# Kernel tuning notes

Measured on AMD Instinct MI355X. Metric: run time of the kernel, lower is better.

The kernel has to match this reference:

```python
import jax, jax.numpy as jnp
import numpy as np

B, T, C = 2, 2048, 2048
NH = 16          # n_head
G = 4            # group_size
NKV = NH // G    # kv heads
HD = C // NH     # head_dim = 128
BASE = 10000.0


def setup_inputs() -> dict:
    key = jax.random.key(0)
    ks = jax.random.split(key, 9)
    s = 0.02
    return {
        "x": jax.random.normal(ks[0], (B, T, C), jnp.float32),
        "wq_w": jax.random.normal(ks[1], (C, C), jnp.float32) * s,
        "wq_b": jax.random.normal(ks[2], (C,), jnp.float32) * s,
        "wk_w": jax.random.normal(ks[3], (C // G, C), jnp.float32) * s,
        "wk_b": jax.random.normal(ks[4], (C // G,), jnp.float32) * s,
        "wv_w": jax.random.normal(ks[5], (C // G, C), jnp.float32) * s,
        "wv_b": jax.random.normal(ks[6], (C // G,), jnp.float32) * s,
        "cp_w": jax.random.normal(ks[7], (C, C), jnp.float32) * s,
        "cp_b": jax.random.normal(ks[8], (C,), jnp.float32) * s,
    }


def _rope(x):
    # Faithful to source: RoPE is applied to [B, H, T, HD] but the module
    # reads seq_len = x.size(1) == H, so the rotation angle is indexed by the
    # HEAD axis and broadcast over sequence positions.
    b, h, t, d = x.shape
    half = d // 2
    theta = 1.0 / (BASE ** (jnp.arange(0, half, dtype=jnp.float32) * 2.0 / d))  # [half]
    ang = jnp.arange(h, dtype=jnp.float32)[:, None] * theta[None, :]            # [h, half]
    cos = jnp.cos(ang)[None, :, None, :]  # [1, h, 1, half]
    sin = jnp.sin(ang)[None, :, None, :]
    xs = x.reshape(b, h, t, half, 2)
    x0, x1 = xs[..., 0], xs[..., 1]
    out = jnp.stack([x0 * cos - x1 * sin, x1 * cos + x0 * sin], axis=-1)
    return out.reshape(b, h, t, d)


def reference(x, wq_w, wq_b, wk_w, wk_b, wv_w, wv_b, cp_w, cp_b):
    b, t, c = x.shape
    q = x @ wq_w.T + wq_b                                  # [B,T,C]
    k = x @ wk_w.T + wk_b                                  # [B,T,C//G]
    v = x @ wv_w.T + wv_b                                  # [B,T,C//G]
    q = q.reshape(b, t, NH, HD).transpose(0, 2, 1, 3)      # [B,NH,T,HD]
    k = k.reshape(b, t, NKV, HD).transpose(0, 2, 1, 3)     # [B,NKV,T,HD]
    v = v.reshape(b, t, NKV, HD).transpose(0, 2, 1, 3)
    q = _rope(q)
    k = _rope(k)
    # GQA expand: each kv head repeated G times consecutively
    k = jnp.repeat(k, G, axis=1)                           # [B,NH,T,HD]
    v = jnp.repeat(v, G, axis=1)
    att = jnp.einsum('bhqd,bhkd->bhqk', q, k) / (HD ** 0.5)
    mask = jnp.tril(jnp.ones((t, t), dtype=bool))
    att = jnp.where(mask[None, None], att, -jnp.inf)
    att = jax.nn.softmax(att, axis=-1)
    y = jnp.einsum('bhqk,bhkd->bhqd', att, v)
    y = y.transpose(0, 2, 1, 3).reshape(b, t, c)
    return y @ cp_w.T + cp_b
```

## Files before the change

kernel.cpp:

```cpp
#include <hip/hip_runtime.h>

typedef unsigned short u16;
typedef __bf16 bf16x8 __attribute__((ext_vector_type(8)));
typedef float f32x4 __attribute__((ext_vector_type(4)));
typedef float f32x16 __attribute__((ext_vector_type(16)));
typedef unsigned u32x4 __attribute__((ext_vector_type(4)));

#define T_   2048
#define C_   2048
#define HD_  128
#define NH_  16
#define NKV_ 4
#define M_   4096

typedef __attribute__((address_space(1))) const void* as1_cvp;
typedef __attribute__((address_space(3))) void* as3_vp;

__device__ __forceinline__ void gload16(const void* g, void* l) {
  __builtin_amdgcn_global_load_lds((as1_cvp)g, (as3_vp)l, 16, 0, 0);
}

__device__ __forceinline__ u16 f2bf(float f) {
  unsigned u = __builtin_bit_cast(unsigned, f);
  return (u16)((u + 0x7fffu + ((u >> 16) & 1u)) >> 16);
}

__device__ __forceinline__ float fexp2(float x) {
  float r;
  asm("v_exp_f32 %0, %1" : "=v"(r) : "v"(x));
  return r;
}

__device__ __forceinline__ unsigned cvtpk(float a, float b) {
  unsigned d;
  asm("v_cvt_pk_bf16_f32 %0, %1, %2" : "=v"(d) : "v"(a), "v"(b));
  return d;
}

__global__ void cvt_bf16(const float4* __restrict__ in, ushort4* __restrict__ out, int n4) {
  int i = blockIdx.x * blockDim.x + threadIdx.x;
  if (i >= n4) return;
  float4 v = in[i];
  ushort4 r;
  r.x = f2bf(v.x); r.y = f2bf(v.y); r.z = f2bf(v.z); r.w = f2bf(v.w);
  out[i] = r;
}

__global__ void copy_f32(const float* __restrict__ in, float* __restrict__ out, int n) {
  int i = blockIdx.x * blockDim.x + threadIdx.x;
  if (i < n) out[i] = in[i];
}

__global__ void rope_fold_w(const float* __restrict__ W, u16* __restrict__ out, int npair) {
  int idx = blockIdx.x * blockDim.x + threadIdx.x;
  int p  = idx >> 9;
  int c4 = (idx & 511) << 2;
  if (p >= npair) return;
  int h  = p >> 6;
  int ii = p & 63;
  float theta = __expf(-(float)ii * (9.210340371976184f / 64.0f));
  float s, c;
  __sincosf((float)h * theta, &s, &c);
  size_t r0 = (size_t)(2 * p) * 2048 + c4;
  size_t r1 = r0 + 2048;
  float4 a = *(const float4*)(W + r0);
  float4 b = *(const float4*)(W + r1);
  ushort4 o0, o1;
  o0.x = f2bf(a.x * c - b.x * s); o0.y = f2bf(a.y * c - b.y * s);
  o0.z = f2bf(a.z * c - b.z * s); o0.w = f2bf(a.w * c - b.w * s);
  o1.x = f2bf(b.x * c + a.x * s); o1.y = f2bf(b.y * c + a.y * s);
  o1.z = f2bf(b.z * c + a.z * s); o1.w = f2bf(b.w * c + a.w * s);
  *(ushort4*)(out + r0) = o0;
  *(ushort4*)(out + r1) = o1;
}

__global__ void rope_fold_b(const float* __restrict__ bin, float* __restrict__ bout, int npair) {
  int p = blockIdx.x * blockDim.x + threadIdx.x;
  if (p >= npair) return;
  int h = p >> 6, ii = p & 63;
  float theta = __expf(-(float)ii * (9.210340371976184f / 64.0f));
  float s, c;
  __sincosf((float)h * theta, &s, &c);
  float a = bin[2 * p], b = bin[2 * p + 1];
  bout[2 * p]     = a * c - b * s;
  bout[2 * p + 1] = b * c + a * s;
}

template<int BN, int MODE>
__global__ __launch_bounds__(512)
void gemm11(const u16* __restrict__ A, const u16* __restrict__ W,
            const float* __restrict__ bias, void* __restrict__ op0,
            void* __restrict__ op1, void* __restrict__ op2, const float qscale) {
  constexpr int NREP = BN / 32;
  constexpr int ABUF = 16384;
  constexpr int BBUF = BN * 64;
  constexpr int NBL  = BN / 64;
  __shared__ __align__(16) u16 sm[3 * ABUF + 2 * BBUF];
  const int tid  = threadIdx.x;
  const int lane = tid & 63;
  const int wid  = tid >> 6;
  const int wr = wid >> 1, wc = wid & 1;
  const int m0 = blockIdx.y << 8;
  const int n0 = blockIdx.x * BN;
  const int K  = C_;
  const int fr = lane & 15, g = lane >> 4;
  const int rs0 = ((g ^ (fr & 7)) << 3);
  const int rs1 = (((4 + g) ^ (fr & 7)) << 3);

  size_t sofA[4]; int sdstA[4];
#pragma unroll
  for (int l = 0; l < 4; ++l) {
    const int j = l * 512 + tid, rl = j >> 3, sl = j & 7;
    sofA[l] = (size_t)rl * K + ((sl ^ (rl & 7)) << 3);
    sdstA[l] = j * 8;
  }
  size_t sofB[NBL]; int sdstB[NBL];
#pragma unroll
  for (int l = 0; l < NBL; ++l) {
    const int j = l * 512 + tid, rl = j >> 3, sl = j & 7;
    sofB[l] = (size_t)rl * K + ((sl ^ (rl & 7)) << 3);
    sdstB[l] = j * 8;
  }
  const u16* Ab = A + (size_t)m0 * K;
  const u16* Bb = W + (size_t)n0 * K;

  f32x4 acc[4][NREP] = {};

#define SA(l, ks, buf) gload16(Ab + (size_t)(ks) * 64 + sofA[l], sm + (buf) * ABUF + sdstA[l]);
#define SB(l, ks, buf) gload16(Bb + (size_t)(ks) * 64 + sofB[l], sm + 3 * ABUF + (buf) * BBUF + sdstB[l]);

#pragma unroll
  for (int l = 0; l < NBL; ++l) SB(l, 0, 0)
#pragma unroll
  for (int l = 0; l < 4; ++l) SA(l, 0, 0)
#pragma unroll
  for (int l = 0; l < 4; ++l) SA(l, 1, 1)
  asm volatile("s_waitcnt vmcnt(4)" ::: "memory");
  __builtin_amdgcn_s_barrier();
  __builtin_amdgcn_sched_barrier(0);

  int a0 = 0, a2 = 2;
  for (int s = 0; s < 32; ++s) {
    const int ab = a0 * ABUF;
    const int bb = 3 * ABUF + (s & 1) * BBUF;
    const int b1 = (s & 1) ^ 1;
    bf16x8 af0[4], af1[4], bq0[NREP], bq1[NREP];
#pragma unroll
    for (int ni = 0; ni < NREP; ++ni)
      bq0[ni] = *(const bf16x8*)&sm[bb + (wc * (BN / 2) + ni * 16 + fr) * 64 + rs0];
#pragma unroll
    for (int mi = 0; mi < 4; ++mi)
      af0[mi] = *(const bf16x8*)&sm[ab + (wr * 64 + mi * 16 + fr) * 64 + rs0];
#pragma unroll
    for (int ni = 0; ni < NREP; ++ni)
      bq1[ni] = *(const bf16x8*)&sm[bb + (wc * (BN / 2) + ni * 16 + fr) * 64 + rs1];
#pragma unroll
    for (int mi = 0; mi < 4; ++mi)
      af1[mi] = *(const bf16x8*)&sm[ab + (wr * 64 + mi * 16 + fr) * 64 + rs1];
    if (s < 31) {
#pragma unroll
      for (int l = 0; l < NBL; ++l) SB(l, s + 1, b1)
    }
    if (s < 30) {
#pragma unroll
      for (int l = 0; l < 4; ++l) SA(l, s + 2, a2)
    }
    __builtin_amdgcn_s_setprio(1);
#pragma unroll
    for (int mi = 0; mi < 4; ++mi)
#pragma unroll
      for (int ni = 0; ni < NREP; ++ni)
        acc[mi][ni] = __builtin_amdgcn_mfma_f32_16x16x32_bf16(af0[mi], bq0[ni], acc[mi][ni], 0, 0, 0);
#pragma unroll
    for (int mi = 0; mi < 4; ++mi)
#pragma unroll
      for (int ni = 0; ni < NREP; ++ni)
        acc[mi][ni] = __builtin_amdgcn_mfma_f32_16x16x32_bf16(af1[mi], bq1[ni], acc[mi][ni], 0, 0, 0);
    __builtin_amdgcn_s_setprio(0);
    if (s < 30)       asm volatile("s_waitcnt vmcnt(4)" ::: "memory");
    else if (s == 30) asm volatile("s_waitcnt vmcnt(0)" ::: "memory");
    if (s < 31) {
      __builtin_amdgcn_s_barrier();
      __builtin_amdgcn_sched_barrier(0);
    }
    a0 = (a0 == 2) ? 0 : a0 + 1;
    a2 = (a2 == 2) ? 0 : a2 + 1;
  }
#undef SA
#undef SB

#pragma unroll
  for (int mi = 0; mi < 4; ++mi) {
    const int rg0 = m0 + wr * 64 + mi * 16 + ((lane >> 4) << 2);
#pragma unroll
    for (int ni = 0; ni < NREP; ++ni) {
      const int cg = n0 + wc * (BN / 2) + ni * 16 + fr;
      const float bb2 = bias[cg];
#pragma unroll
      for (int r = 0; r < 4; ++r) {
        float v = acc[mi][ni][r] + bb2;
        const int rg = rg0 + r;
        if (MODE == 1) {
          ((float*)op0)[(size_t)rg * C_ + cg] = v;
        } else {
          const int b = rg >> 11, t = rg & (T_ - 1);
          if (cg < 2048) {
            const int h = cg >> 7, d = cg & 127;
            ((u16*)op0)[((((size_t)b * NH_ + h) * T_ + t) << 7) + d] = f2bf(v * qscale);
          } else if (cg < 2560) {
            const int c2 = cg - 2048, h = c2 >> 7, d = c2 & 127;
            ((u16*)op1)[((((size_t)b * NKV_ + h) * T_ + t) << 7) + d] = f2bf(v);
          } else {
            const int c2 = cg - 2560, h = c2 >> 7, d = c2 & 127;
            ((u16*)op2)[(((size_t)b * NKV_ + h) * HD_ + d) * T_ + t] = f2bf(v);
          }
        }
      }
    }
  }
}

__device__ __forceinline__ void stage_kv(u16* dst, const u16* __restrict__ kg,
                                         const u16* __restrict__ vg, int lane, int w) {
#pragma unroll
  for (int r = 0; r < 4; ++r) {
    const int row = r * 16 + w * 4 + (lane >> 4);
    const int cg  = (lane & 15) ^ (row & 7);
    gload16(kg + (size_t)row * 128 + cg * 8, dst + row * 128 + (lane & 15) * 8);
  }
#pragma unroll
  for (int r = 0; r < 4; ++r) {
    const int row = r * 32 + w * 8 + (lane >> 3);
    const int cg  = (lane & 7) ^ (row & 7);
    gload16(vg + (size_t)row * T_ + cg * 8, dst + 8192 + row * 64 + (lane & 7) * 8);
  }
}

__global__ __launch_bounds__(256, 2)
void attn2(const u16* __restrict__ q, const u16* __restrict__ k,
           const u16* __restrict__ vt, u16* __restrict__ y) {
  __shared__ __align__(16) u16 sm[32768];
  const int tid  = threadIdx.x;
  const int lane = tid & 63;
  const int w    = tid >> 6;
  const int hi   = lane >> 5;
  const int l5   = lane & 31;
  const int h = blockIdx.y;
  const int b = blockIdx.z;
  const int qt = b ? (int)blockIdx.x : (15 - (int)blockIdx.x);
  const int q0  = qt << 7;
  const int q0w = q0 + w * 32;
  const int nkv = 2 * qt + 2;
  const size_t qbase = (((size_t)b * NH_ + h) * T_ + q0) * HD_;
  const size_t kbase = ((size_t)b * NKV_ + (h >> 2)) * (size_t)T_ * HD_;
  const size_t vbase = ((size_t)b * NKV_ + (h >> 2)) * (size_t)HD_ * T_;

#pragma unroll
  for (int r = 0; r < 8; ++r) {
    const int row = r * 16 + w * 4 + (lane >> 4);
    const int cg  = (lane & 15) ^ (row & 7);
    gload16(q + qbase + (size_t)row * 128 + cg * 8, sm + row * 128 + (lane & 15) * 8);
  }
  __syncthreads();
  bf16x8 qf[8];
  {
    const int row = w * 32 + l5;
#pragma unroll
    for (int kd = 0; kd < 8; ++kd)
      qf[kd] = *(const bf16x8*)&sm[row * 128 + ((((kd << 1) | hi) ^ (row & 7)) << 3)];
  }
  __syncthreads();
  stage_kv(sm, k + kbase, vt + vbase, lane, w);

  f32x16 o[4] = {};
  float m = -1e30f, l = 0.f;

  for (int kv = 0; kv < nkv; ++kv) {
    __syncthreads();
    const int buf = kv & 1;
    if (kv + 1 < nkv)
      stage_kv(sm + ((buf ^ 1) << 14),
               k + kbase + ((size_t)(kv + 1) << 6) * 128,
               vt + vbase + ((kv + 1) << 6), lane, w);

    if ((kv << 6) <= q0w + 31) {
      const u16* Ks = sm + (buf << 14);
      const u16* Vs = Ks + 8192;

      f32x16 st[2] = {};
      __builtin_amdgcn_s_setprio(1);
#pragma unroll
      for (int kt = 0; kt < 2; ++kt) {
        const int krow = kt * 32 + l5;
#pragma unroll
        for (int kd = 0; kd < 8; ++kd) {
          bf16x8 ka = *(const bf16x8*)&Ks[krow * 128 + ((((kd << 1) | hi) ^ (l5 & 7)) << 3)];
          st[kt] = __builtin_amdgcn_mfma_f32_32x32x16_bf16(ka, qf[kd], st[kt], 0, 0, 0);
        }
      }
      __builtin_amdgcn_s_setprio(0);

      if ((kv << 6) + 63 > q0w) {
        const int qg = q0w + l5;
#pragma unroll
        for (int kt = 0; kt < 2; ++kt)
#pragma unroll
          for (int r = 0; r < 16; ++r) {
            const int kg = (kv << 6) + kt * 32 + (r & 3) + ((r >> 2) << 3) + (hi << 2);
            if (kg > qg) st[kt][r] = -3.0e38f;
          }
      }

      float pmax = -3.0e38f;
#pragma unroll
      for (int kt = 0; kt < 2; ++kt)
#pragma unroll
        for (int r = 0; r < 16; ++r) pmax = fmaxf(pmax, st[kt][r]);
      pmax = fmaxf(pmax, __shfl_xor(pmax, 32));
      if (!__all(pmax - m <= 8.0f)) {
        const float mn = fmaxf(m, pmax);
        const float f = fexp2(m - mn);
        m = mn;
        l *= f;
#pragma unroll
        for (int r = 0; r < 16; ++r) {
          const float fr = __shfl(f, (r & 3) + ((r >> 2) << 3) + (hi << 2));
          o[0][r] *= fr; o[1][r] *= fr; o[2][r] *= fr; o[3][r] *= fr;
        }
      }

      float rs = 0.f;
#pragma unroll
      for (int kt = 0; kt < 2; ++kt) {
#pragma unroll
        for (int s = 0; s < 2; ++s) {
          float e0 = fexp2(st[kt][8 * s + 0] - m), e1 = fexp2(st[kt][8 * s + 1] - m);
          float e2 = fexp2(st[kt][8 * s + 2] - m), e3 = fexp2(st[kt][8 * s + 3] - m);
          float e4 = fexp2(st[kt][8 * s + 4] - m), e5 = fexp2(st[kt][8 * s + 5] - m);
          float e6 = fexp2(st[kt][8 * s + 6] - m), e7 = fexp2(st[kt][8 * s + 7] - m);
          rs += ((e0 + e1) + (e2 + e3)) + ((e4 + e5) + (e6 + e7));
          const unsigned wL0 = cvtpk(e0, e1), wL1 = cvtpk(e2, e3);
          const unsigned wH0 = cvtpk(e4, e5), wH1 = cvtpk(e6, e7);
          const unsigned s0 = hi ? wL0 : wH0, s1 = hi ? wL1 : wH1;
          const unsigned r0 = __shfl_xor(s0, 32), r1 = __shfl_xor(s1, 32);
          u32x4 fw;
          fw.x = hi ? r0 : wL0; fw.y = hi ? r1 : wL1;
          fw.z = hi ? wH0 : r0; fw.w = hi ? wH1 : r1;
          const bf16x8 pa = __builtin_bit_cast(bf16x8, fw);
          const int ch = (((kt * 2 + s) << 1) | hi) ^ (l5 & 7);
          __builtin_amdgcn_s_setprio(1);
#pragma unroll
          for (int ds = 0; ds < 4; ++ds) {
            const int vrow = ds * 32 + l5;
            bf16x8 vb = *(const bf16x8*)&Vs[vrow * 64 + (ch << 3)];
            o[ds] = __builtin_amdgcn_mfma_f32_32x32x16_bf16(pa, vb, o[ds], 0, 0, 0);
          }
          __builtin_amdgcn_s_setprio(0);
        }
      }
      rs += __shfl_xor(rs, 32);
      l += rs;
    }
  }

  const float linv = 1.0f / l;
#pragma unroll
  for (int r = 0; r < 16; ++r) {
    const int crow = (r & 3) + ((r >> 2) << 3) + (hi << 2);
    const float lf = __shfl(linv, crow);
    const int qg = q0w + crow;
    const size_t rowoff = (((size_t)(b << 11) + qg) << 11) + (h << 7) + l5;
#pragma unroll
    for (int ds = 0; ds < 4; ++ds)
      y[rowoff + ds * 32] = f2bf(o[ds][r] * lf);
  }
}

extern "C" void kernel_launch(void* const* d_in, const int* in_sizes, int n_in,
                              void* d_out, int out_size, void* d_ws, size_t ws_size,
                              hipStream_t stream) {
  (void)in_sizes; (void)n_in; (void)out_size; (void)ws_size;
  const float* x    = (const float*)d_in[0];
  const float* wq_w = (const float*)d_in[1];
  const float* wq_b = (const float*)d_in[2];
  const float* wk_w = (const float*)d_in[3];
  const float* wk_b = (const float*)d_in[4];
  const float* wv_w = (const float*)d_in[5];
  const float* wv_b = (const float*)d_in[6];
  const float* cp_w = (const float*)d_in[7];
  const float* cp_b = (const float*)d_in[8];

  char* ws = (char*)d_ws;
  u16* xb  = (u16*)ws;  ws += (size_t)M_ * C_ * 2;
  u16* wqr = (u16*)ws;  ws += (size_t)C_ * C_ * 2;
  u16* wkr = (u16*)ws;  ws += (size_t)512 * C_ * 2;
  u16* wvb = (u16*)ws;  ws += (size_t)512 * C_ * 2;
  u16* cpb = (u16*)ws;  ws += (size_t)C_ * C_ * 2;
  u16* qb  = (u16*)ws;  ws += (size_t)M_ * C_ * 2;
  u16* kb  = (u16*)ws;  ws += (size_t)M_ * 512 * 2;
  u16* vtb = (u16*)ws;  ws += (size_t)M_ * 512 * 2;
  float* bqkv = (float*)ws; ws += 3072 * 4;
  u16* yb = xb;

  cvt_bf16<<<8192, 256, 0, stream>>>((const float4*)x,    (ushort4*)xb,  2097152);
  cvt_bf16<<<1024, 256, 0, stream>>>((const float4*)wv_w, (ushort4*)wvb, 262144);
  cvt_bf16<<<4096, 256, 0, stream>>>((const float4*)cp_w, (ushort4*)cpb, 1048576);
  rope_fold_w<<<2048, 256, 0, stream>>>(wq_w, wqr, 1024);
  rope_fold_w<<<512,  256, 0, stream>>>(wk_w, wkr, 256);
  rope_fold_b<<<4, 256, 0, stream>>>(wq_b, bqkv, 1024);
  rope_fold_b<<<1, 256, 0, stream>>>(wk_b, bqkv + 2048, 256);
  copy_f32<<<2, 256, 0, stream>>>(wv_b, bqkv + 2560, 512);

  const float qscale = 0.08838834764831843f * 1.4426950408889634f;
  gemm11<192, 0><<<dim3(16, 16), 512, 0, stream>>>(xb, wqr, bqkv, qb, kb, vtb, qscale);

  attn2<<<dim3(16, 16, 2), 256, 0, stream>>>(qb, kb, vtb, yb);

  gemm11<128, 1><<<dim3(16, 16), 512, 0, stream>>>(yb, cpb, cp_b, (float*)d_out,
                                                   nullptr, nullptr, 1.0f);
}
```

Baseline: 187.1 us.

## Restructure GEMM to 128-row tiles with A fragments loaded directly to registers

The projection GEMMs move from 256-row tiles with 512 threads and LDS-staged A to 128-row tiles with 256 threads. A fragments are now read straight from global memory into double-buffered registers, and only B is staged through LDS. This shrinks LDS use and doubles the grid, aiming for better occupancy and less LDS traffic, at the cost of uncoalesced, non-shared A reads from global. The small prep kernels are also merged (wv and cp conversion in one kernel, all bias preparation in one kernel) to cut launch count.

```diff
diff --git a/kernel.cpp b/kernel.cpp
--- a/kernel.cpp
+++ b/kernel.cpp
@@ -46,9 +46,16 @@
   out[i] = r;
 }
 
-__global__ void copy_f32(const float* __restrict__ in, float* __restrict__ out, int n) {
+__global__ void cvt_wvcp(const float4* __restrict__ wv, const float4* __restrict__ cp,
+                         ushort4* __restrict__ wvb, ushort4* __restrict__ cpb) {
   int i = blockIdx.x * blockDim.x + threadIdx.x;
-  if (i < n) out[i] = in[i];
+  const float4* src; ushort4* dst; int j;
+  if (i < 262144) { src = wv; dst = wvb; j = i; }
+  else            { src = cp; dst = cpb; j = i - 262144; }
+  float4 v = src[j];
+  ushort4 r;
+  r.x = f2bf(v.x); r.y = f2bf(v.y); r.z = f2bf(v.z); r.w = f2bf(v.w);
+  dst[j] = r;
 }
 
 __global__ void rope_fold_w(const float* __restrict__ W, u16* __restrict__ out, int npair) {
@@ -74,120 +81,119 @@
   *(ushort4*)(out + r1) = o1;
 }
 
-__global__ void rope_fold_b(const float* __restrict__ bin, float* __restrict__ bout, int npair) {
-  int p = blockIdx.x * blockDim.x + threadIdx.x;
-  if (p >= npair) return;
-  int h = p >> 6, ii = p & 63;
-  float theta = __expf(-(float)ii * (9.210340371976184f / 64.0f));
-  float s, c;
-  __sincosf((float)h * theta, &s, &c);
-  float a = bin[2 * p], b = bin[2 * p + 1];
-  bout[2 * p]     = a * c - b * s;
-  bout[2 * p + 1] = b * c + a * s;
+__global__ void prep_bias(const float* __restrict__ wq_b, const float* __restrict__ wk_b,
+                          const float* __restrict__ wv_b, float* __restrict__ bqkv) {
+  int i = blockIdx.x * blockDim.x + threadIdx.x;
+  if (i < 1280) {
+    const float* src = (i < 1024) ? wq_b : wk_b;
+    float* dst = (i < 1024) ? bqkv : (bqkv + 2048);
+    int p = (i < 1024) ? i : (i - 1024);
+    int ii = p & 63;
+    float theta = __expf(-(float)ii * (9.210340371976184f / 64.0f));
+    float s, c;
+    __sincosf((float)(p >> 6) * theta, &s, &c);
+    float a = src[2 * p], b = src[2 * p + 1];
+    dst[2 * p]     = a * c - b * s;
+    dst[2 * p + 1] = b * c + a * s;
+  } else if (i < 1536) {
+    int p = i - 1280;
+    bqkv[2560 + 2 * p]     = wv_b[2 * p];
+    bqkv[2560 + 2 * p + 1] = wv_b[2 * p + 1];
+  }
 }
 
 template<int BN, int MODE>
-__global__ __launch_bounds__(512)
-void gemm11(const u16* __restrict__ A, const u16* __restrict__ W,
+__global__ __launch_bounds__(256)
+void gemm13(const u16* __restrict__ A, const u16* __restrict__ W,
             const float* __restrict__ bias, void* __restrict__ op0,
             void* __restrict__ op1, void* __restrict__ op2, const float qscale) {
   constexpr int NREP = BN / 32;
-  constexpr int ABUF = 16384;
   constexpr int BBUF = BN * 64;
-  constexpr int NBL  = BN / 64;
-  __shared__ __align__(16) u16 sm[3 * ABUF + 2 * BBUF];
+  constexpr int NBL  = BN / 32;
+  __shared__ __align__(16) u16 sm[2 * BBUF];
   const int tid  = threadIdx.x;
   const int lane = tid & 63;
   const int wid  = tid >> 6;
   const int wr = wid >> 1, wc = wid & 1;
-  const int m0 = blockIdx.y << 8;
+  const int m0 = blockIdx.y << 7;
   const int n0 = blockIdx.x * BN;
   const int K  = C_;
   const int fr = lane & 15, g = lane >> 4;
   const int rs0 = ((g ^ (fr & 7)) << 3);
   const int rs1 = (((4 + g) ^ (fr & 7)) << 3);
 
-  size_t sofA[4]; int sdstA[4];
-#pragma unroll
-  for (int l = 0; l < 4; ++l) {
-    const int j = l * 512 + tid, rl = j >> 3, sl = j & 7;
-    sofA[l] = (size_t)rl * K + ((sl ^ (rl & 7)) << 3);
-    sdstA[l] = j * 8;
-  }
-  size_t sofB[NBL]; int sdstB[NBL];
+  const u16* srcB[NBL]; int dstB[NBL];
 #pragma unroll
   for (int l = 0; l < NBL; ++l) {
-    const int j = l * 512 + tid, rl = j >> 3, sl = j & 7;
-    sofB[l] = (size_t)rl * K + ((sl ^ (rl & 7)) << 3);
-    sdstB[l] = j * 8;
-  }
-  const u16* Ab = A + (size_t)m0 * K;
-  const u16* Bb = W + (size_t)n0 * K;
+    const int j = l * 256 + tid, row = j >> 3, sl = j & 7;
+    srcB[l] = W + (size_t)(n0 + row) * K + ((sl ^ (row & 7)) << 3);
+    dstB[l] = j * 8;
+  }
+  const u16* ap[4];
+#pragma unroll
+  for (int mi = 0; mi < 4; ++mi)
+    ap[mi] = A + (size_t)(m0 + wr * 64 + mi * 16 + fr) * K + g * 8;
 
   f32x4 acc[4][NREP] = {};
-
-#define SA(l, ks, buf) gload16(Ab + (size_t)(ks) * 64 + sofA[l], sm + (buf) * ABUF + sdstA[l]);
-#define SB(l, ks, buf) gload16(Bb + (size_t)(ks) * 64 + sofB[l], sm + 3 * ABUF + (buf) * BBUF + sdstB[l]);
-
-#pragma unroll
-  for (int l = 0; l < NBL; ++l) SB(l, 0, 0)
-#pragma unroll
-  for (int l = 0; l < 4; ++l) SA(l, 0, 0)
-#pragma unroll
-  for (int l = 0; l < 4; ++l) SA(l, 1, 1)
-  asm volatile("s_waitcnt vmcnt(4)" ::: "memory");
+  bf16x8 afA[4][2], afB[4][2];
+
+#pragma unroll
+  for (int l = 0; l < NBL; ++l) gload16(srcB[l], sm + dstB[l]);
+#pragma unroll
+  for (int mi = 0; mi < 4; ++mi)
+#pragma unroll
+    for (int kh = 0; kh < 2; ++kh)
+      afA[mi][kh] = *(const bf16x8*)(ap[mi] + kh * 32);
+  asm volatile("s_waitcnt vmcnt(8)" ::: "memory");
   __builtin_amdgcn_s_barrier();
   __builtin_amdgcn_sched_barrier(0);
 
-  int a0 = 0, a2 = 2;
-  for (int s = 0; s < 32; ++s) {
-    const int ab = a0 * ABUF;
-    const int bb = 3 * ABUF + (s & 1) * BBUF;
-    const int b1 = (s & 1) ^ 1;
-    bf16x8 af0[4], af1[4], bq0[NREP], bq1[NREP];
-#pragma unroll
-    for (int ni = 0; ni < NREP; ++ni)
-      bq0[ni] = *(const bf16x8*)&sm[bb + (wc * (BN / 2) + ni * 16 + fr) * 64 + rs0];
-#pragma unroll
-    for (int mi = 0; mi < 4; ++mi)
-      af0[mi] = *(const bf16x8*)&sm[ab + (wr * 64 + mi * 16 + fr) * 64 + rs0];
-#pragma unroll
-    for (int ni = 0; ni < NREP; ++ni)
-      bq1[ni] = *(const bf16x8*)&sm[bb + (wc * (BN / 2) + ni * 16 + fr) * 64 + rs1];
-#pragma unroll
-    for (int mi = 0; mi < 4; ++mi)
-      af1[mi] = *(const bf16x8*)&sm[ab + (wr * 64 + mi * 16 + fr) * 64 + rs1];
-    if (s < 31) {
-#pragma unroll
-      for (int l = 0; l < NBL; ++l) SB(l, s + 1, b1)
-    }
-    if (s < 30) {
-#pragma unroll
-      for (int l = 0; l < 4; ++l) SA(l, s + 2, a2)
-    }
-    __builtin_amdgcn_s_setprio(1);
-#pragma unroll
-    for (int mi = 0; mi < 4; ++mi)
-#pragma unroll
-      for (int ni = 0; ni < NREP; ++ni)
-        acc[mi][ni] = __builtin_amdgcn_mfma_f32_16x16x32_bf16(af0[mi], bq0[ni], acc[mi][ni], 0, 0, 0);
-#pragma unroll
-    for (int mi = 0; mi < 4; ++mi)
-#pragma unroll
-      for (int ni = 0; ni < NREP; ++ni)
-        acc[mi][ni] = __builtin_amdgcn_mfma_f32_16x16x32_bf16(af1[mi], bq1[ni], acc[mi][ni], 0, 0, 0);
-    __builtin_amdgcn_s_setprio(0);
-    if (s < 30)       asm volatile("s_waitcnt vmcnt(4)" ::: "memory");
-    else if (s == 30) asm volatile("s_waitcnt vmcnt(0)" ::: "memory");
-    if (s < 31) {
-      __builtin_amdgcn_s_barrier();
-      __builtin_amdgcn_sched_barrier(0);
-    }
-    a0 = (a0 == 2) ? 0 : a0 + 1;
-    a2 = (a2 == 2) ? 0 : a2 + 1;
-  }
-#undef SA
-#undef SB
+#define STEP(s, afC, afN) {                                                   \
+    const int bb = ((s) & 1) * BBUF;                                          \
+    bf16x8 bq0[NREP], bq1[NREP];                                              \
+    _Pragma("unroll")                                                         \
+    for (int ni = 0; ni < NREP; ++ni) {                                       \
+      const int row = wc * (BN / 2) + ni * 16 + fr;                           \
+      bq0[ni] = *(const bf16x8*)&sm[bb + row * 64 + rs0];                     \
+      bq1[ni] = *(const bf16x8*)&sm[bb + row * 64 + rs1];                     \
+    }                                                                         \
+    if ((s) < 31) {                                                           \
+      _Pragma("unroll")                                                       \
+      for (int l = 0; l < NBL; ++l)                                           \
+        gload16(srcB[l] + ((s) + 1) * 64, sm + (((s) & 1) ^ 1) * BBUF + dstB[l]); \
+      _Pragma("unroll")                                                       \
+      for (int mi = 0; mi < 4; ++mi)                                          \
+        _Pragma("unroll")                                                     \
+        for (int kh = 0; kh < 2; ++kh)                                        \
+          afN[mi][kh] = *(const bf16x8*)(ap[mi] + ((s) + 1) * 64 + kh * 32);  \
+    }                                                                         \
+    __builtin_amdgcn_s_setprio(1);                                            \
+    _Pragma("unroll")                                                         \
+    for (int mi = 0; mi < 4; ++mi)                                            \
+      _Pragma("unroll")                                                       \
+      for (int ni = 0; ni < NREP; ++ni)                                       \
+        acc[mi][ni] = __builtin_amdgcn_mfma_f32_16x16x32_bf16(                \
+            afC[mi][0], bq0[ni], acc[mi][ni], 0, 0, 0);                       \
+    _Pragma("unroll")                                                         \
+    for (int mi = 0; mi < 4; ++mi)                                            \
+      _Pragma("unroll")                                                       \
+      for (int ni = 0; ni < NREP; ++ni)                                       \
+        acc[mi][ni] = __builtin_amdgcn_mfma_f32_16x16x32_bf16(                \
+            afC[mi][1], bq1[ni], acc[mi][ni], 0, 0, 0);                       \
+    __builtin_amdgcn_s_setprio(0);                                            \
+    if ((s) < 31) {                                                           \
+      asm volatile("s_waitcnt vmcnt(8)" ::: "memory");                        \
+      __builtin_amdgcn_s_barrier();                                           \
+      __builtin_amdgcn_sched_barrier(0);                                      \
+    }                                                                         \
+  }
+
+#pragma unroll 1
+  for (int sp = 0; sp < 16; ++sp) {
+    STEP(2 * sp,     afA, afB)
+    STEP(2 * sp + 1, afB, afA)
+  }
+#undef STEP
 
 #pragma unroll
   for (int mi = 0; mi < 4; ++mi) {
@@ -402,20 +408,18 @@
   float* bqkv = (float*)ws; ws += 3072 * 4;
   u16* yb = xb;
 
-  cvt_bf16<<<8192, 256, 0, stream>>>((const float4*)x,    (ushort4*)xb,  2097152);
-  cvt_bf16<<<1024, 256, 0, stream>>>((const float4*)wv_w, (ushort4*)wvb, 262144);
-  cvt_bf16<<<4096, 256, 0, stream>>>((const float4*)cp_w, (ushort4*)cpb, 1048576);
+  cvt_bf16<<<8192, 256, 0, stream>>>((const float4*)x, (ushort4*)xb, 2097152);
+  cvt_wvcp<<<5120, 256, 0, stream>>>((const float4*)wv_w, (const float4*)cp_w,
+                                     (ushort4*)wvb, (ushort4*)cpb);
   rope_fold_w<<<2048, 256, 0, stream>>>(wq_w, wqr, 1024);
   rope_fold_w<<<512,  256, 0, stream>>>(wk_w, wkr, 256);
-  rope_fold_b<<<4, 256, 0, stream>>>(wq_b, bqkv, 1024);
-  rope_fold_b<<<1, 256, 0, stream>>>(wk_b, bqkv + 2048, 256);
-  copy_f32<<<2, 256, 0, stream>>>(wv_b, bqkv + 2560, 512);
+  prep_bias<<<6, 256, 0, stream>>>(wq_b, wk_b, wv_b, bqkv);
 
   const float qscale = 0.08838834764831843f * 1.4426950408889634f;
-  gemm11<192, 0><<<dim3(16, 16), 512, 0, stream>>>(xb, wqr, bqkv, qb, kb, vtb, qscale);
+  gemm13<192, 0><<<dim3(16, 32), 256, 0, stream>>>(xb, wqr, bqkv, qb, kb, vtb, qscale);
 
   attn2<<<dim3(16, 16, 2), 256, 0, stream>>>(qb, kb, vtb, yb);
 
-  gemm11<128, 1><<<dim3(16, 16), 512, 0, stream>>>(yb, cpb, cp_b, (float*)d_out,
+  gemm13<128, 1><<<dim3(16, 32), 256, 0, stream>>>(yb, cpb, cp_b, (float*)d_out,
                                                    nullptr, nullptr, 1.0f);
 }
```

Result: slower. 281.8 us (+50.6%).
